# Performance work log

Hardware: AMD Instinct MI355X
Metric: run time of the kernel (lower is better)

## Reference

```python
import jax, jax.numpy as jnp
import numpy as np

B, S, E = 8, 2048, 1024
EPS = 1e-5

def _layernorm(x, w, b):
    mu = jnp.mean(x, axis=-1, keepdims=True)
    var = jnp.mean(jnp.square(x - mu), axis=-1, keepdims=True)
    return (x - mu) * jax.lax.rsqrt(var + EPS) * w + b

def setup_inputs() -> dict:
    key = jax.random.key(0)
    ks = jax.random.split(key, 12)
    x = jax.random.normal(ks[0], (B, S, E), dtype=jnp.float32)
    pad_mask = jax.random.randint(ks[1], (B, 1, S), 0, 2).astype(bool)
    pad_mask = pad_mask.at[:, :, 0].set(False)  # ensure no fully-masked row
    s = 1.0 / np.sqrt(E)
    Wq = jax.random.normal(ks[2], (E, E), jnp.float32) * s
    Wk = jax.random.normal(ks[3], (E, E), jnp.float32) * s
    Wv = jax.random.normal(ks[4], (E, E), jnp.float32) * s
    bq = jnp.zeros((E,), jnp.float32)
    bk = jnp.zeros((E,), jnp.float32)
    bv = jnp.zeros((E,), jnp.float32)
    W1 = jax.random.normal(ks[5], (2 * E, E), jnp.float32) * s
    b1 = jnp.zeros((2 * E,), jnp.float32)
    W2 = jax.random.normal(ks[6], (E, 2 * E), jnp.float32) * (1.0 / np.sqrt(2 * E))
    b2 = jnp.zeros((E,), jnp.float32)
    ln1_w = jnp.ones((E,), jnp.float32); ln1_b = jnp.zeros((E,), jnp.float32)
    ln2_w = jnp.ones((E,), jnp.float32); ln2_b = jnp.zeros((E,), jnp.float32)
    return {"x": x, "pad_mask": pad_mask, "ln1_w": ln1_w, "ln1_b": ln1_b,
            "ln2_w": ln2_w, "ln2_b": ln2_b, "Wq": Wq, "bq": bq, "Wk": Wk,
            "bk": bk, "Wv": Wv, "bv": bv, "W1": W1, "b1": b1, "W2": W2, "b2": b2}

def reference(x, pad_mask, ln1_w, ln1_b, ln2_w, ln2_b, Wq, bq, Wk, bk, Wv, bv, W1, b1, W2, b2):
    scale = jnp.sqrt(jnp.float32(x.shape[-1]))
    normed = _layernorm(x, ln1_w, ln1_b)
    Q = jnp.einsum('bse,de->bsd', normed, Wq) + bq
    K = jnp.einsum('bse,de->bsd', normed, Wk) + bk
    V = jnp.einsum('bse,de->bsd', normed, Wv) + bv
    scores = jnp.einsum('bqd,bkd->bqk', Q, K) / scale  # [B,S,S]
    scores = jnp.where(pad_mask, -jnp.inf, scores)
    attn = jax.nn.softmax(scores, axis=2)  # dropout is identity at inference
    x = x + jnp.einsum('bqk,bkd->bqd', attn, V)
    h = _layernorm(x, ln2_w, ln2_b)
    h = jax.nn.relu(jnp.einsum('bse,fe->bsf', h, W1) + b1)
    x = x + jnp.einsum('bsf,ef->bse', h, W2) + b2
    return x
```

## Files before the change

kernel.cpp:

```cpp
#include <hip/hip_runtime.h>
#include <hip/hip_bf16.h>
#include <cstdint>

#define B_ 8
#define S_ 2048
#define E_ 1024

using u16 = unsigned short;

typedef __bf16 bf16x8 __attribute__((ext_vector_type(8)));
typedef float f32x4 __attribute__((ext_vector_type(4)));

__device__ inline u16 f2bf(float f) {
  uint32_t u = __float_as_uint(f);
  uint32_t r = (u + 0x7fffu + ((u >> 16) & 1u)) >> 16;
  return (u16)r;
}

template<bool HAS_BIAS, bool RELU, bool HAS_RES, bool OUT_BF16, bool SCORES,
         bool GATHER_A, bool RUNTK>
__global__ __launch_bounds__(256) void gemm_nt(
    const u16* __restrict__ A, const u16* __restrict__ B, void* __restrict__ C,
    const float* __restrict__ bias, const float* __restrict__ res,
    int lda, int ldb, int ldc, int K,
    long long strideA, long long strideB, long long strideC,
    const int* __restrict__ cidx, const int* __restrict__ cnt)
{
  __shared__ u16 lA[128 * 32];
  __shared__ u16 lB[128 * 32];

  const int tid  = threadIdx.x;
  const int lane = tid & 63;
  const int wave = tid >> 6;

  const int GM = 4, GN = 8;
  const int nbn = gridDim.x, nbm = gridDim.y, nz = gridDim.z;
  int bm, bn, bz;
  {
    const int total = nbn * nbm * nz;
    const long long lin = blockIdx.x +
        (long long)nbn * (blockIdx.y + (long long)nbm * blockIdx.z);
    if ((nbm % GM) == 0 && (nbn % GN) == 0 && (total % (8 * GM * GN)) == 0) {
      const int xcd = (int)(lin & 7);
      const int loc = (int)(lin >> 3);
      const int sper = GM * GN;
      const int super = (loc / sper) * 8 + xcd;
      const int ins   = loc % sper;
      const int spz = (nbm / GM) * (nbn / GN);
      bz = super / spz;
      const int s2 = super % spz;
      const int sm = s2 % (nbm / GM);
      const int sn = s2 / (nbm / GM);
      bm = sm * GM + (ins % GM);
      bn = sn * GN + (ins / GM);
    } else { bm = blockIdx.y; bn = blockIdx.x; bz = blockIdx.z; }
  }

  int count = 0, cpad = 0;
  if (SCORES || GATHER_A || RUNTK) {
    count = cnt[bz * 2];
    cpad  = cnt[bz * 2 + 1];
    if (GATHER_A && bm * 128 >= cpad) return;
    if (SCORES   && bn * 128 >= cpad) return;
  }
  const int Keff = RUNTK ? cpad : K;

  const u16* Ab = A + (long long)bz * strideA;
  const u16* Bb = B + (long long)bz * strideB;

  const bool stageA = (wave < 2);
  const int  wpart  = (wave & 1) * 64;
  const int  srow   = lane >> 2;
  const int  scol   = (lane & 3) * 8;
  const int  ld     = stageA ? lda : ldb;

  long long goff[4];
  if (GATHER_A && stageA) {
    const int* cx = cidx;
#pragma unroll
    for (int c = 0; c < 4; ++c) {
      const int r = cx[(long long)bz * S_ + bm * 128 + wpart + 16 * c + srow];
      goff[c] = (long long)r * lda + scol;
    }
  } else {
    const int rbase = (stageA ? bm : bn) * 128 + wpart + srow;
#pragma unroll
    for (int c = 0; c < 4; ++c)
      goff[c] = (long long)(rbase + 16 * c) * ld + scol;
  }
  const u16* gb = stageA ? Ab : Bb;
  u16* ldst = (stageA ? lA : lB) + wpart * 32;

  f32x4 acc[4][4];
#pragma unroll
  for (int i = 0; i < 4; ++i)
#pragma unroll
    for (int j = 0; j < 4; ++j)
      acc[i][j] = (f32x4){0.f, 0.f, 0.f, 0.f};

  const int wm = (wave >> 1) * 64;
  const int wn = (wave & 1) * 64;
  const u16* pA = lA + (wm + (lane & 15)) * 32 + (lane >> 4) * 8;
  const u16* pB = lB + (wn + (lane & 15)) * 32 + (lane >> 4) * 8;

  const int nk = Keff >> 5;
  for (int kt = 0; kt < nk; ++kt) {
    __syncthreads();
#pragma unroll
    for (int c = 0; c < 4; ++c) {
      __builtin_amdgcn_global_load_lds(
          (const __attribute__((address_space(1))) void*)(gb + goff[c] + kt * 32),
          (__attribute__((address_space(3))) void*)(ldst + c * 16 * 32),
          16, 0, 0);
    }
    __syncthreads();

    bf16x8 af[4], bfr[4];
#pragma unroll
    for (int i = 0; i < 4; ++i) af[i] = *(const bf16x8*)(pA + i * 16 * 32);
#pragma unroll
    for (int j = 0; j < 4; ++j) bfr[j] = *(const bf16x8*)(pB + j * 16 * 32);
#pragma unroll
    for (int i = 0; i < 4; ++i)
#pragma unroll
      for (int j = 0; j < 4; ++j)
        acc[i][j] = __builtin_amdgcn_mfma_f32_16x16x32_bf16(af[i], bfr[j], acc[i][j], 0, 0, 0);
  }

  const int rb = wm + (lane >> 4) * 4;
  const int cb = wn + (lane & 15);
  const float* resb = (const float*)C;
  if (HAS_RES) resb = res + (long long)bz * strideC;
  u16*   cb16 = (u16*)C   + (long long)bz * strideC;
  float* cf32 = (float*)C + (long long)bz * strideC;

#pragma unroll
  for (int j = 0; j < 4; ++j) {
    const int gn = bn * 128 + cb + j * 16;
    const float bvv = HAS_BIAS ? bias[gn] : 0.f;
    const bool cmask = SCORES && (gn >= count);
#pragma unroll
    for (int i = 0; i < 4; ++i) {
#pragma unroll
      for (int r = 0; r < 4; ++r) {
        const int gm = bm * 128 + rb + i * 16 + r;
        const long long idx = (long long)gm * ldc + gn;
        float v = acc[i][j][r] + bvv;
        if (SCORES) { v *= 0.03125f; if (cmask) v = -3.0e38f; }
        if (RELU) v = fmaxf(v, 0.f);
        if (HAS_RES) v += resb[idx];
        if (OUT_BF16) cb16[idx] = f2bf(v);
        else          cf32[idx] = v;
      }
    }
  }
}

__global__ __launch_bounds__(256) void layernorm_kernel(
    const float* __restrict__ x, const float* __restrict__ w,
    const float* __restrict__ b, u16* __restrict__ out)
{
  const int row = blockIdx.x;
  const int tid = threadIdx.x;
  const float4 v = ((const float4*)(x + (long long)row * E_))[tid];
  float s  = v.x + v.y + v.z + v.w;
  float s2 = v.x * v.x + v.y * v.y + v.z * v.z + v.w * v.w;
#pragma unroll
  for (int o = 32; o >= 1; o >>= 1) { s += __shfl_xor(s, o); s2 += __shfl_xor(s2, o); }
  __shared__ float rs[4], rs2[4];
  const int wave = tid >> 6, lane = tid & 63;
  if (lane == 0) { rs[wave] = s; rs2[wave] = s2; }
  __syncthreads();
  s  = rs[0] + rs[1] + rs[2] + rs[3];
  s2 = rs2[0] + rs2[1] + rs2[2] + rs2[3];
  const float mu   = s * (1.f / E_);
  const float var  = s2 * (1.f / E_) - mu * mu;
  const float rstd = rsqrtf(var + 1e-5f);
  const float4 wv = ((const float4*)w)[tid];
  const float4 bv = ((const float4*)b)[tid];
  ushort4 o;
  o.x = f2bf((v.x - mu) * rstd * wv.x + bv.x);
  o.y = f2bf((v.y - mu) * rstd * wv.y + bv.y);
  o.z = f2bf((v.z - mu) * rstd * wv.z + bv.z);
  o.w = f2bf((v.w - mu) * rstd * wv.w + bv.w);
  ((ushort4*)(out + (long long)row * E_))[tid] = o;
}

__global__ __launch_bounds__(256) void softmax_bf16_kernel(
    u16* __restrict__ sp, const int* __restrict__ cnt)
{
  const int row = blockIdx.x;
  const int bz  = row >> 11;
  const int tid = threadIdx.x;
  const int cpad = cnt[bz * 2 + 1];
  const bool act = (tid * 8) < cpad;
  u16* pr = sp + (long long)row * S_;

  float v[8];
  if (act) {
    const uint4 raw = ((const uint4*)pr)[tid];
    const uint32_t w[4] = {raw.x, raw.y, raw.z, raw.w};
#pragma unroll
    for (int c = 0; c < 4; ++c) {
      v[2 * c]     = __uint_as_float(w[c] << 16);
      v[2 * c + 1] = __uint_as_float(w[c] & 0xffff0000u);
    }
  } else {
#pragma unroll
    for (int i = 0; i < 8; ++i) v[i] = -3.38e38f;
  }
  float mx = -3.38e38f;
#pragma unroll
  for (int i = 0; i < 8; ++i) mx = fmaxf(mx, v[i]);
#pragma unroll
  for (int o = 32; o >= 1; o >>= 1) mx = fmaxf(mx, __shfl_xor(mx, o));
  __shared__ float red[4];
  const int wave = tid >> 6, lane = tid & 63;
  if (lane == 0) red[wave] = mx;
  __syncthreads();
  mx = fmaxf(fmaxf(red[0], red[1]), fmaxf(red[2], red[3]));

  float s = 0.f;
#pragma unroll
  for (int i = 0; i < 8; ++i) { v[i] = __expf(v[i] - mx); s += v[i]; }
#pragma unroll
  for (int o = 32; o >= 1; o >>= 1) s += __shfl_xor(s, o);
  __syncthreads();
  if (lane == 0) red[wave] = s;
  __syncthreads();
  s = red[0] + red[1] + red[2] + red[3];
  const float inv = 1.f / s;

  if (act) {
    uint4 o4;
    uint32_t* ow = (uint32_t*)&o4;
#pragma unroll
    for (int c = 0; c < 4; ++c) {
      const uint32_t lo = f2bf(v[2 * c] * inv);
      const uint32_t hi = f2bf(v[2 * c + 1] * inv);
      ow[c] = lo | (hi << 16);
    }
    ((uint4*)pr)[tid] = o4;
  }
}

__global__ __launch_bounds__(256) void transpose_kernel(
    const u16* __restrict__ KVc, u16* __restrict__ Vt, const int* __restrict__ cnt)
{
  const int bl = blockIdx.z;
  const int s0 = blockIdx.y * 32;
  if (s0 >= cnt[bl * 2 + 1]) return;
  __shared__ u16 tile[32][33];
  const int e0 = blockIdx.x * 32;
  const int tx = threadIdx.x & 31, ty = threadIdx.x >> 5;
  const u16* src = KVc + ((long long)bl * S_ + s0) * (2 * E_) + E_ + e0;
#pragma unroll
  for (int r = 0; r < 32; r += 8)
    tile[ty + r][tx] = src[(long long)(ty + r) * (2 * E_) + tx];
  __syncthreads();
  u16* dst = Vt + ((long long)bl * E_ + e0) * S_ + s0;
#pragma unroll
  for (int r = 0; r < 32; r += 8)
    dst[(long long)(ty + r) * S_ + tx] = tile[tx][ty + r];
}

__global__ __launch_bounds__(256) void prep_kernel(
    const float* __restrict__ Wq, const float* __restrict__ Wk,
    const float* __restrict__ Wv, const float* __restrict__ W1,
    const float* __restrict__ W2, const float* __restrict__ bk,
    const float* __restrict__ bv,
    u16* __restrict__ Wqb, u16* __restrict__ Wkvb,
    u16* __restrict__ W1b, u16* __restrict__ W2b, float* __restrict__ bkv)
{
  const int N1 = E_ * E_;
  const long long i = (long long)blockIdx.x * 256 + threadIdx.x;
  if (i < N1)               Wqb[i] = f2bf(Wq[i]);
  else if (i < 2LL * N1)    Wkvb[i - N1] = f2bf(Wk[i - N1]);
  else if (i < 3LL * N1)    Wkvb[N1 + (i - 2LL * N1)] = f2bf(Wv[i - 2LL * N1]);
  else if (i < 5LL * N1)    W1b[i - 3LL * N1] = f2bf(W1[i - 3LL * N1]);
  else if (i < 7LL * N1)    W2b[i - 5LL * N1] = f2bf(W2[i - 5LL * N1]);
  else if (i < 7LL * N1 + 2 * E_) {
    const int j = (int)(i - 7LL * N1);
    bkv[j] = (j < E_) ? bk[j] : bv[j - E_];
  }
}

__global__ void detect_kernel(const unsigned char* __restrict__ m, int* __restrict__ flag)
{
  __shared__ int any;
  if (threadIdx.x == 0) any = 0;
  __syncthreads();
  int loc = 0;
  for (int i = threadIdx.x; i < B_ * S_; i += 256)
    if ((i & 3) && m[i]) loc = 1;
  if (loc) atomicOr(&any, 1);
  __syncthreads();
  if (threadIdx.x == 0) *flag = any;
}

__global__ __launch_bounds__(256) void compact_kernel(
    const void* __restrict__ mask, const int* __restrict__ flag,
    int* __restrict__ cidx, int* __restrict__ cnt)
{
  const int b = blockIdx.x;
  const int tid = threadIdx.x, lane = tid & 63, wave = tid >> 6;
  const bool u8m = (*flag != 0);
  const unsigned char* m8 = (const unsigned char*)mask + (long long)b * S_;
  const int* m32 = (const int*)mask + (long long)b * S_;

  int keep[8]; int my = 0;
#pragma unroll
  for (int j = 0; j < 8; ++j) {
    const int s = tid * 8 + j;
    const bool k = u8m ? (m8[s] == 0) : (m32[s] == 0);
    keep[j] = k ? 1 : 0; my += keep[j];
  }
  int pre = my;
#pragma unroll
  for (int o = 1; o < 64; o <<= 1) {
    const int n = __shfl_up(pre, o);
    if (lane >= o) pre += n;
  }
  __shared__ int wsum[4];
  if (lane == 63) wsum[wave] = pre;
  __syncthreads();
  int wbase = 0;
#pragma unroll
  for (int w = 0; w < 4; ++w) if (w < wave) wbase += wsum[w];
  int pos = wbase + pre - my;
  int* cx = cidx + (long long)b * S_;
#pragma unroll
  for (int j = 0; j < 8; ++j)
    if (keep[j]) cx[pos++] = tid * 8 + j;
  const int total = wsum[0] + wsum[1] + wsum[2] + wsum[3];
  const int cpad = (total + 127) & ~127;
  for (int i = total + tid; i < cpad; i += 256) cx[i] = 0;
  if (tid == 0) { cnt[b * 2] = total; cnt[b * 2 + 1] = cpad; }
}

extern "C" void kernel_launch(void* const* d_in, const int* in_sizes, int n_in,
                              void* d_out, int out_size, void* d_ws, size_t ws_size,
                              hipStream_t stream)
{
  const float* x    = (const float*)d_in[0];
  const void*  mask = d_in[1];
  const float* ln1w = (const float*)d_in[2];
  const float* ln1b = (const float*)d_in[3];
  const float* ln2w = (const float*)d_in[4];
  const float* ln2b = (const float*)d_in[5];
  const float* Wq   = (const float*)d_in[6];
  const float* bq   = (const float*)d_in[7];
  const float* Wk   = (const float*)d_in[8];
  const float* bk   = (const float*)d_in[9];
  const float* Wv   = (const float*)d_in[10];
  const float* bv   = (const float*)d_in[11];
  const float* W1   = (const float*)d_in[12];
  const float* b1   = (const float*)d_in[13];
  const float* W2   = (const float*)d_in[14];
  const float* b2   = (const float*)d_in[15];

  const size_t MB = 1024ull * 1024ull;
  char* p = (char*)d_ws;
  int* flag    = (int*)p;   p += 256;
  int* cnt     = (int*)p;   p += 256;
  int* cidx    = (int*)p;   p += (size_t)B_ * S_ * 4;
  u16* Wqb     = (u16*)p;   p += (size_t)E_ * E_ * 2;
  u16* Wkvb    = (u16*)p;   p += (size_t)2 * E_ * E_ * 2;
  u16* W1b     = (u16*)p;   p += (size_t)2 * E_ * E_ * 2;
  u16* W2b     = (u16*)p;   p += (size_t)2 * E_ * E_ * 2;
  float* bkv   = (float*)p; p += 2 * E_ * 4;
  u16* normedb = (u16*)p;   p += (size_t)B_ * S_ * E_ * 2;
  char* chunk  = p;
  const size_t used  = (size_t)(p - (char*)d_ws);
  const size_t avail = (ws_size > used) ? (ws_size - used) : 0;

  int bc = 1;
  for (int c = 8; c >= 1; c >>= 1)
    if (avail >= 24 * MB * (size_t)c) { bc = c; break; }

  float* out = (float*)d_out;
  dim3 blk(256);

  detect_kernel<<<1, 256, 0, stream>>>((const unsigned char*)mask, flag);
  compact_kernel<<<B_, blk, 0, stream>>>(mask, flag, cidx, cnt);
  {
    const long long tot = 7LL * E_ * E_ + 2 * E_;
    prep_kernel<<<(int)((tot + 255) / 256), blk, 0, stream>>>(
        Wq, Wk, Wv, W1, W2, bk, bv, Wqb, Wkvb, W1b, W2b, bkv);
  }

  layernorm_kernel<<<B_ * S_, blk, 0, stream>>>(x, ln1w, ln1b, normedb);

  for (int b0 = 0; b0 < B_; b0 += bc) {
    u16* Qc  = (u16*)chunk;
    u16* KVc = Qc + (size_t)bc * S_ * E_;
    u16* Vt  = KVc + (size_t)bc * S_ * 2 * E_;
    u16* Pc  = Vt + (size_t)bc * E_ * S_;
    const int* cntb  = cnt + b0 * 2;
    const int* cidxb = cidx + (size_t)b0 * S_;

    gemm_nt<true, false, false, true, false, false, false>
        <<<dim3(E_ / 128, bc * S_ / 128, 1), blk, 0, stream>>>(
        normedb + (size_t)b0 * S_ * E_, Wqb, Qc, bq, nullptr,
        E_, E_, E_, E_, 0, 0, 0, nullptr, nullptr);

    gemm_nt<true, false, false, true, false, true, false>
        <<<dim3(2 * E_ / 128, S_ / 128, bc), blk, 0, stream>>>(
        normedb + (size_t)b0 * S_ * E_, Wkvb, KVc, bkv, nullptr,
        E_, E_, 2 * E_, E_,
        (long long)S_ * E_, 0, (long long)S_ * 2 * E_, cidxb, cntb);

    transpose_kernel<<<dim3(E_ / 32, S_ / 32, bc), blk, 0, stream>>>(KVc, Vt, cntb);

    gemm_nt<false, false, false, true, true, false, false>
        <<<dim3(S_ / 128, S_ / 128, bc), blk, 0, stream>>>(
        Qc, KVc, Pc, nullptr, nullptr,
        E_, 2 * E_, S_, E_,
        (long long)S_ * E_, (long long)S_ * 2 * E_, (long long)S_ * S_,
        nullptr, cntb);

    softmax_bf16_kernel<<<bc * S_, blk, 0, stream>>>(Pc, cntb);

    gemm_nt<false, false, true, false, false, false, true>
        <<<dim3(E_ / 128, S_ / 128, bc), blk, 0, stream>>>(
        Pc, Vt, out + (size_t)b0 * S_ * E_, nullptr,
        x + (size_t)b0 * S_ * E_, S_, S_, E_, S_,
        (long long)S_ * S_, (long long)E_ * S_, (long long)S_ * E_,
        nullptr, cntb);
  }

  layernorm_kernel<<<B_ * S_, blk, 0, stream>>>(out, ln2w, ln2b, normedb);

  size_t mr_sz = avail / ((size_t)2 * E_ * 2);
  int mr = (int)((mr_sz > 16384) ? 16384 : mr_sz);
  mr &= ~127;
  if (mr < 128) mr = 128;
  u16* hb = (u16*)chunk;
  for (int m0 = 0; m0 < B_ * S_; m0 += mr) {
    const int mm = (B_ * S_ - m0 < mr) ? (B_ * S_ - m0) : mr;
    gemm_nt<true, true, false, true, false, false, false>
        <<<dim3((2 * E_) / 128, mm / 128, 1), blk, 0, stream>>>(
        normedb + (size_t)m0 * E_, W1b, hb, b1, nullptr,
        E_, E_, 2 * E_, E_, 0, 0, 0, nullptr, nullptr);
    gemm_nt<true, false, true, false, false, false, false>
        <<<dim3(E_ / 128, mm / 128, 1), blk, 0, stream>>>(
        hb, W2b, out + (size_t)m0 * E_, b2, out + (size_t)m0 * E_,
        2 * E_, 2 * E_, E_, 2 * E_, 0, 0, 0, nullptr, nullptr);
  }
}
```

Measured before the change: 778.1 us.

## Rewrite GEMM as 256x256 tile, 512-thread, double-buffered pipelined kernel with swizzled LDS

Replaces the 128x128x32 single-buffered GEMM with a 256x256x64 tile computed by 8 waves. LDS is double-buffered and XOR-swizzled, and global-to-LDS loads are interleaved with four MFMA phases using explicit barriers, waitcnt and setprio. The goal is higher arithmetic intensity, fewer bank conflicts and overlap of memory traffic with MFMA work. Padding for the compacted key count grows to 256, and all launch grids change to match. The cost is much higher LDS and register use, fewer blocks, and more wasted padding work.

```diff
diff --git a/kernel.cpp b/kernel.cpp
--- a/kernel.cpp
+++ b/kernel.cpp
@@ -19,21 +19,21 @@
 
 template<bool HAS_BIAS, bool RELU, bool HAS_RES, bool OUT_BF16, bool SCORES,
          bool GATHER_A, bool RUNTK>
-__global__ __launch_bounds__(256) void gemm_nt(
+__global__ __launch_bounds__(512, 2) void gemm_nt(
     const u16* __restrict__ A, const u16* __restrict__ B, void* __restrict__ C,
     const float* __restrict__ bias, const float* __restrict__ res,
     int lda, int ldb, int ldc, int K,
     long long strideA, long long strideB, long long strideC,
     const int* __restrict__ cidx, const int* __restrict__ cnt)
 {
-  __shared__ u16 lA[128 * 32];
-  __shared__ u16 lB[128 * 32];
+  __shared__ __attribute__((aligned(16))) u16 lA[2][2][128 * 64];
+  __shared__ __attribute__((aligned(16))) u16 lB[2][2][128 * 64];
 
   const int tid  = threadIdx.x;
   const int lane = tid & 63;
   const int wave = tid >> 6;
 
-  const int GM = 4, GN = 8;
+  const int GM = 8, GN = 4;
   const int nbn = gridDim.x, nbm = gridDim.y, nz = gridDim.z;
   int bm, bn, bz;
   {
@@ -60,92 +60,139 @@
   if (SCORES || GATHER_A || RUNTK) {
     count = cnt[bz * 2];
     cpad  = cnt[bz * 2 + 1];
-    if (GATHER_A && bm * 128 >= cpad) return;
-    if (SCORES   && bn * 128 >= cpad) return;
+    if (GATHER_A && bm * 256 >= cpad) return;
+    if (SCORES   && bn * 256 >= cpad) return;
   }
   const int Keff = RUNTK ? cpad : K;
+  const int nk = Keff >> 6;
 
   const u16* Ab = A + (long long)bz * strideA;
   const u16* Bb = B + (long long)bz * strideB;
 
-  const bool stageA = (wave < 2);
-  const int  wpart  = (wave & 1) * 64;
-  const int  srow   = lane >> 2;
-  const int  scol   = (lane & 3) * 8;
-  const int  ld     = stageA ? lda : ldb;
-
-  long long goff[4];
-  if (GATHER_A && stageA) {
-    const int* cx = cidx;
-#pragma unroll
-    for (int c = 0; c < 4; ++c) {
-      const int r = cx[(long long)bz * S_ + bm * 128 + wpart + 16 * c + srow];
-      goff[c] = (long long)r * lda + scol;
+  const int srow = tid >> 3;
+  const int scol = ((tid & 7) ^ (srow & 7)) * 8;
+  long long rowA[2][2], rowB[2][2];
+#pragma unroll
+  for (int h = 0; h < 2; ++h)
+#pragma unroll
+    for (int l = 0; l < 2; ++l) {
+      int ra = bm * 256 + h * 128 + srow + l * 64;
+      if (GATHER_A) ra = cidx[(long long)bz * S_ + ra];
+      rowA[h][l] = (long long)ra * lda + scol;
+      rowB[h][l] = (long long)(bn * 256 + h * 128 + srow + l * 64) * ldb + scol;
     }
-  } else {
-    const int rbase = (stageA ? bm : bn) * 128 + wpart + srow;
-#pragma unroll
-    for (int c = 0; c < 4; ++c)
-      goff[c] = (long long)(rbase + 16 * c) * ld + scol;
-  }
-  const u16* gb = stageA ? Ab : Bb;
-  u16* ldst = (stageA ? lA : lB) + wpart * 32;
-
-  f32x4 acc[4][4];
-#pragma unroll
-  for (int i = 0; i < 4; ++i)
-#pragma unroll
-    for (int j = 0; j < 4; ++j)
-      acc[i][j] = (f32x4){0.f, 0.f, 0.f, 0.f};
-
-  const int wm = (wave >> 1) * 64;
-  const int wn = (wave & 1) * 64;
-  const u16* pA = lA + (wm + (lane & 15)) * 32 + (lane >> 4) * 8;
-  const u16* pB = lB + (wn + (lane & 15)) * 32 + (lane >> 4) * 8;
-
-  const int nk = Keff >> 5;
-  for (int kt = 0; kt < nk; ++kt) {
-    __syncthreads();
-#pragma unroll
-    for (int c = 0; c < 4; ++c) {
-      __builtin_amdgcn_global_load_lds(
-          (const __attribute__((address_space(1))) void*)(gb + goff[c] + kt * 32),
-          (__attribute__((address_space(3))) void*)(ldst + c * 16 * 32),
-          16, 0, 0);
-    }
-    __syncthreads();
-
-    bf16x8 af[4], bfr[4];
-#pragma unroll
-    for (int i = 0; i < 4; ++i) af[i] = *(const bf16x8*)(pA + i * 16 * 32);
-#pragma unroll
-    for (int j = 0; j < 4; ++j) bfr[j] = *(const bf16x8*)(pB + j * 16 * 32);
-#pragma unroll
-    for (int i = 0; i < 4; ++i)
-#pragma unroll
-      for (int j = 0; j < 4; ++j)
-        acc[i][j] = __builtin_amdgcn_mfma_f32_16x16x32_bf16(af[i], bfr[j], acc[i][j], 0, 0, 0);
-  }
-
-  const int rb = wm + (lane >> 4) * 4;
-  const int cb = wn + (lane & 15);
+  const int ldsoff0 = tid * 8;
+  const int ldsoff1 = (tid + 512) * 8;
+
+  const int wr = wave >> 2, wc = wave & 3;
+  const int rA = wr * 64 + (lane & 15);
+  const int rB = wc * 32 + (lane & 15);
+  int aoff[2], boff[2];
+#pragma unroll
+  for (int k2 = 0; k2 < 2; ++k2) {
+    aoff[k2] = rA * 64 + (((k2 * 4 + (lane >> 4)) ^ (rA & 7)) * 8);
+    boff[k2] = rB * 64 + (((k2 * 4 + (lane >> 4)) ^ (rB & 7)) * 8);
+  }
+
+  f32x4 acc[2][2][4][2];
+#pragma unroll
+  for (int a = 0; a < 2; ++a)
+#pragma unroll
+    for (int b = 0; b < 2; ++b)
+#pragma unroll
+      for (int mi = 0; mi < 4; ++mi)
+#pragma unroll
+        for (int ni = 0; ni < 2; ++ni)
+          acc[a][b][mi][ni] = (f32x4){0.f, 0.f, 0.f, 0.f};
+
+#define STAGE_A(H, T) {                                                        \
+    const int tt_ = ((T) < nk) ? (T) : (nk - 1);                               \
+    __builtin_amdgcn_global_load_lds(                                          \
+        (const __attribute__((address_space(1))) void*)                        \
+            (Ab + rowA[H][0] + (long long)tt_ * 64),                           \
+        (__attribute__((address_space(3))) void*)(&lA[(T) & 1][H][ldsoff0]),   \
+        16, 0, 0);                                                             \
+    __builtin_amdgcn_global_load_lds(                                          \
+        (const __attribute__((address_space(1))) void*)                        \
+            (Ab + rowA[H][1] + (long long)tt_ * 64),                           \
+        (__attribute__((address_space(3))) void*)(&lA[(T) & 1][H][ldsoff1]),   \
+        16, 0, 0); }
+
+#define STAGE_B(H, T) {                                                        \
+    const int tt_ = ((T) < nk) ? (T) : (nk - 1);                               \
+    __builtin_amdgcn_global_load_lds(                                          \
+        (const __attribute__((address_space(1))) void*)                        \
+            (Bb + rowB[H][0] + (long long)tt_ * 64),                           \
+        (__attribute__((address_space(3))) void*)(&lB[(T) & 1][H][ldsoff0]),   \
+        16, 0, 0);                                                             \
+    __builtin_amdgcn_global_load_lds(                                          \
+        (const __attribute__((address_space(1))) void*)                        \
+            (Bb + rowB[H][1] + (long long)tt_ * 64),                           \
+        (__attribute__((address_space(3))) void*)(&lB[(T) & 1][H][ldsoff1]),   \
+        16, 0, 0); }
+
+#define PHASE(MH, NH, STG, DO_VM) {                                            \
+    bf16x8 af[4][2], bfv[2][2];                                                \
+    const u16* pa_ = &lA[buf][MH][0];                                          \
+    const u16* pb_ = &lB[buf][NH][0];                                          \
+    _Pragma("unroll") for (int mi = 0; mi < 4; ++mi)                           \
+      _Pragma("unroll") for (int k2 = 0; k2 < 2; ++k2)                         \
+        af[mi][k2] = *(const bf16x8*)(pa_ + mi * 1024 + aoff[k2]);             \
+    _Pragma("unroll") for (int ni = 0; ni < 2; ++ni)                           \
+      _Pragma("unroll") for (int k2 = 0; k2 < 2; ++k2)                         \
+        bfv[ni][k2] = *(const bf16x8*)(pb_ + ni * 1024 + boff[k2]);            \
+    STG;                                                                       \
+    __builtin_amdgcn_s_barrier();                                              \
+    asm volatile("s_waitcnt lgkmcnt(0)" ::: "memory");                         \
+    __builtin_amdgcn_s_setprio(1);                                             \
+    _Pragma("unroll") for (int mi = 0; mi < 4; ++mi)                           \
+      _Pragma("unroll") for (int ni = 0; ni < 2; ++ni)                         \
+        _Pragma("unroll") for (int k2 = 0; k2 < 2; ++k2)                       \
+          acc[MH][NH][mi][ni] = __builtin_amdgcn_mfma_f32_16x16x32_bf16(       \
+              af[mi][k2], bfv[ni][k2], acc[MH][NH][mi][ni], 0, 0, 0);          \
+    __builtin_amdgcn_s_setprio(0);                                             \
+    if (DO_VM) asm volatile("s_waitcnt vmcnt(4)" ::: "memory");                \
+    __builtin_amdgcn_s_barrier(); }
+
+  STAGE_A(0, 0); STAGE_B(0, 0); STAGE_A(1, 0); STAGE_B(1, 0);
+  STAGE_A(0, 1); STAGE_B(1, 1);
+  asm volatile("s_waitcnt vmcnt(4)" ::: "memory");
+  __builtin_amdgcn_s_barrier();
+
+  int buf = 0;
+  for (int t = 0; t < nk; ++t, buf ^= 1) {
+    PHASE(0, 0, STAGE_A(1, t + 1), false)
+    PHASE(0, 1, STAGE_B(0, t + 1), false)
+    PHASE(1, 1, STAGE_A(0, t + 2), false)
+    PHASE(1, 0, STAGE_B(1, t + 2), true)
+  }
+  asm volatile("s_waitcnt vmcnt(0)" ::: "memory");
+
+#undef PHASE
+#undef STAGE_A
+#undef STAGE_B
+
   const float* resb = (const float*)C;
   if (HAS_RES) resb = res + (long long)bz * strideC;
   u16*   cb16 = (u16*)C   + (long long)bz * strideC;
   float* cf32 = (float*)C + (long long)bz * strideC;
 
 #pragma unroll
-  for (int j = 0; j < 4; ++j) {
-    const int gn = bn * 128 + cb + j * 16;
+  for (int mh = 0; mh < 2; ++mh)
+#pragma unroll
+  for (int nh = 0; nh < 2; ++nh)
+#pragma unroll
+  for (int ni = 0; ni < 2; ++ni) {
+    const int gn = bn * 256 + nh * 128 + wc * 32 + ni * 16 + (lane & 15);
     const float bvv = HAS_BIAS ? bias[gn] : 0.f;
     const bool cmask = SCORES && (gn >= count);
 #pragma unroll
-    for (int i = 0; i < 4; ++i) {
+    for (int mi = 0; mi < 4; ++mi) {
 #pragma unroll
       for (int r = 0; r < 4; ++r) {
-        const int gm = bm * 128 + rb + i * 16 + r;
+        const int gm = bm * 256 + mh * 128 + wr * 64 + mi * 16 + (lane >> 4) * 4 + r;
         const long long idx = (long long)gm * ldc + gn;
-        float v = acc[i][j][r] + bvv;
+        float v = acc[mh][nh][mi][ni][r] + bvv;
         if (SCORES) { v *= 0.03125f; if (cmask) v = -3.0e38f; }
         if (RELU) v = fmaxf(v, 0.f);
         if (HAS_RES) v += resb[idx];
@@ -333,7 +380,7 @@
   for (int j = 0; j < 8; ++j)
     if (keep[j]) cx[pos++] = tid * 8 + j;
   const int total = wsum[0] + wsum[1] + wsum[2] + wsum[3];
-  const int cpad = (total + 127) & ~127;
+  const int cpad = (total + 255) & ~255;
   for (int i = total + tid; i < cpad; i += 256) cx[i] = 0;
   if (tid == 0) { cnt[b * 2] = total; cnt[b * 2 + 1] = cpad; }
 }
@@ -380,6 +427,7 @@
 
   float* out = (float*)d_out;
   dim3 blk(256);
+  dim3 blkg(512);
 
   detect_kernel<<<1, 256, 0, stream>>>((const unsigned char*)mask, flag);
   compact_kernel<<<B_, blk, 0, stream>>>(mask, flag, cidx, cnt);
@@ -400,12 +448,12 @@
     const int* cidxb = cidx + (size_t)b0 * S_;
 
     gemm_nt<true, false, false, true, false, false, false>
-        <<<dim3(E_ / 128, bc * S_ / 128, 1), blk, 0, stream>>>(
+        <<<dim3(E_ / 256, bc * S_ / 256, 1), blkg, 0, stream>>>(
         normedb + (size_t)b0 * S_ * E_, Wqb, Qc, bq, nullptr,
         E_, E_, E_, E_, 0, 0, 0, nullptr, nullptr);
 
     gemm_nt<true, false, false, true, false, true, false>
-        <<<dim3(2 * E_ / 128, S_ / 128, bc), blk, 0, stream>>>(
+        <<<dim3(2 * E_ / 256, S_ / 256, bc), blkg, 0, stream>>>(
         normedb + (size_t)b0 * S_ * E_, Wkvb, KVc, bkv, nullptr,
         E_, E_, 2 * E_, E_,
         (long long)S_ * E_, 0, (long long)S_ * 2 * E_, cidxb, cntb);
@@ -413,7 +461,7 @@
     transpose_kernel<<<dim3(E_ / 32, S_ / 32, bc), blk, 0, stream>>>(KVc, Vt, cntb);
 
     gemm_nt<false, false, false, true, true, false, false>
-        <<<dim3(S_ / 128, S_ / 128, bc), blk, 0, stream>>>(
+        <<<dim3(S_ / 256, S_ / 256, bc), blkg, 0, stream>>>(
         Qc, KVc, Pc, nullptr, nullptr,
         E_, 2 * E_, S_, E_,
         (long long)S_ * E_, (long long)S_ * 2 * E_, (long long)S_ * S_,
@@ -422,7 +470,7 @@
     softmax_bf16_kernel<<<bc * S_, blk, 0, stream>>>(Pc, cntb);
 
     gemm_nt<false, false, true, false, false, false, true>
-        <<<dim3(E_ / 128, S_ / 128, bc), blk, 0, stream>>>(
+        <<<dim3(E_ / 256, S_ / 256, bc), blkg, 0, stream>>>(
         Pc, Vt, out + (size_t)b0 * S_ * E_, nullptr,
         x + (size_t)b0 * S_ * E_, S_, S_, E_, S_,
         (long long)S_ * S_, (long long)E_ * S_, (long long)S_ * E_,
@@ -433,17 +481,17 @@
 
   size_t mr_sz = avail / ((size_t)2 * E_ * 2);
   int mr = (int)((mr_sz > 16384) ? 16384 : mr_sz);
-  mr &= ~127;
-  if (mr < 128) mr = 128;
+  mr &= ~255;
+  if (mr < 256) mr = 256;
   u16* hb = (u16*)chunk;
   for (int m0 = 0; m0 < B_ * S_; m0 += mr) {
     const int mm = (B_ * S_ - m0 < mr) ? (B_ * S_ - m0) : mr;
     gemm_nt<true, true, false, true, false, false, false>
-        <<<dim3((2 * E_) / 128, mm / 128, 1), blk, 0, stream>>>(
+        <<<dim3((2 * E_) / 256, mm / 256, 1), blkg, 0, stream>>>(
         normedb + (size_t)m0 * E_, W1b, hb, b1, nullptr,
         E_, E_, 2 * E_, E_, 0, 0, 0, nullptr, nullptr);
     gemm_nt<true, false, true, false, false, false, false>
-        <<<dim3(E_ / 128, mm / 128, 1), blk, 0, stream>>>(
+        <<<dim3(E_ / 256, mm / 256, 1), blkg, 0, stream>>>(
         hb, W2b, out + (size_t)m0 * E_, b2, out + (size_t)m0 * E_,
         2 * E_, 2 * E_, E_, 2 * E_, 0, 0, 0, nullptr, nullptr);
   }
```

New measurement: 718.1 us. 7.7% less time.

## Double-buffer GEMM LDS with BK=64, XOR swizzle and hand-scheduled MFMA

Applied to the files above, without the earlier changes.

Rewrites the GEMM main loop to use a K-tile of 64 with two LDS buffers. The next tile is prefetched by global_load_lds while the current one is consumed, which removes one of the two barriers per iteration. LDS columns are XOR-swizzled to avoid bank conflicts, and fragment reads use explicit ds_read_b128 with staged lgkmcnt waits interleaved with the MFMAs. The change also sets launch_bounds occupancy to 2 and swaps the block-grouping shape to 8x4. It adds LDS pressure (64KB per block) and relies on inline asm wait counts being correct.

```diff
diff --git a/kernel.cpp b/kernel.cpp
--- a/kernel.cpp
+++ b/kernel.cpp
@@ -19,21 +19,21 @@
 
 template<bool HAS_BIAS, bool RELU, bool HAS_RES, bool OUT_BF16, bool SCORES,
          bool GATHER_A, bool RUNTK>
-__global__ __launch_bounds__(256) void gemm_nt(
+__global__ __launch_bounds__(256, 2) void gemm_nt(
     const u16* __restrict__ A, const u16* __restrict__ B, void* __restrict__ C,
     const float* __restrict__ bias, const float* __restrict__ res,
     int lda, int ldb, int ldc, int K,
     long long strideA, long long strideB, long long strideC,
     const int* __restrict__ cidx, const int* __restrict__ cnt)
 {
-  __shared__ u16 lA[128 * 32];
-  __shared__ u16 lB[128 * 32];
+  __shared__ __attribute__((aligned(16))) u16 lA[2][128 * 64];
+  __shared__ __attribute__((aligned(16))) u16 lB[2][128 * 64];
 
   const int tid  = threadIdx.x;
   const int lane = tid & 63;
   const int wave = tid >> 6;
 
-  const int GM = 4, GN = 8;
+  const int GM = 8, GN = 4;
   const int nbn = gridDim.x, nbm = gridDim.y, nz = gridDim.z;
   int bm, bn, bz;
   {
@@ -64,88 +64,124 @@
     if (SCORES   && bn * 128 >= cpad) return;
   }
   const int Keff = RUNTK ? cpad : K;
+  const int nk = Keff >> 6;
 
   const u16* Ab = A + (long long)bz * strideA;
   const u16* Bb = B + (long long)bz * strideB;
 
-  const bool stageA = (wave < 2);
-  const int  wpart  = (wave & 1) * 64;
-  const int  srow   = lane >> 2;
-  const int  scol   = (lane & 3) * 8;
-  const int  ld     = stageA ? lda : ldb;
-
-  long long goff[4];
-  if (GATHER_A && stageA) {
-    const int* cx = cidx;
-#pragma unroll
-    for (int c = 0; c < 4; ++c) {
-      const int r = cx[(long long)bz * S_ + bm * 128 + wpart + 16 * c + srow];
-      goff[c] = (long long)r * lda + scol;
-    }
-  } else {
-    const int rbase = (stageA ? bm : bn) * 128 + wpart + srow;
-#pragma unroll
-    for (int c = 0; c < 4; ++c)
-      goff[c] = (long long)(rbase + 16 * c) * ld + scol;
-  }
-  const u16* gb = stageA ? Ab : Bb;
-  u16* ldst = (stageA ? lA : lB) + wpart * 32;
+  const int srow = tid >> 3;
+  const int scol = ((tid & 7) ^ (srow & 7)) * 8;
+  long long rowA[4], rowB[4];
+#pragma unroll
+  for (int l = 0; l < 4; ++l) {
+    int ra = bm * 128 + srow + l * 32;
+    if (GATHER_A) ra = cidx[(long long)bz * S_ + ra];
+    rowA[l] = (long long)ra * lda + scol;
+    rowB[l] = (long long)(bn * 128 + srow + l * 32) * ldb + scol;
+  }
+  const int ldsoff = tid * 8;
+
+  const int wr = wave >> 1, wc = wave & 1;
+  const int rA = wr * 64 + (lane & 15);
+  const int rB = wc * 64 + (lane & 15);
+#define LDSP3(P) ((uint32_t)(uintptr_t)(__attribute__((address_space(3))) const void*)(P))
+  uint32_t aA0 = LDSP3(&lA[0][0]) +
+      2u * (uint32_t)(rA * 64 + (((0 * 4 + (lane >> 4)) ^ (rA & 7)) * 8));
+  uint32_t aA1 = LDSP3(&lA[0][0]) +
+      2u * (uint32_t)(rA * 64 + (((1 * 4 + (lane >> 4)) ^ (rA & 7)) * 8));
+  uint32_t bB0 = LDSP3(&lB[0][0]) +
+      2u * (uint32_t)(rB * 64 + (((0 * 4 + (lane >> 4)) ^ (rB & 7)) * 8));
+  uint32_t bB1 = LDSP3(&lB[0][0]) +
+      2u * (uint32_t)(rB * 64 + (((1 * 4 + (lane >> 4)) ^ (rB & 7)) * 8));
+#undef LDSP3
 
   f32x4 acc[4][4];
 #pragma unroll
-  for (int i = 0; i < 4; ++i)
-#pragma unroll
-    for (int j = 0; j < 4; ++j)
-      acc[i][j] = (f32x4){0.f, 0.f, 0.f, 0.f};
-
-  const int wm = (wave >> 1) * 64;
-  const int wn = (wave & 1) * 64;
-  const u16* pA = lA + (wm + (lane & 15)) * 32 + (lane >> 4) * 8;
-  const u16* pB = lB + (wn + (lane & 15)) * 32 + (lane >> 4) * 8;
-
-  const int nk = Keff >> 5;
-  for (int kt = 0; kt < nk; ++kt) {
-    __syncthreads();
-#pragma unroll
-    for (int c = 0; c < 4; ++c) {
-      __builtin_amdgcn_global_load_lds(
-          (const __attribute__((address_space(1))) void*)(gb + goff[c] + kt * 32),
-          (__attribute__((address_space(3))) void*)(ldst + c * 16 * 32),
-          16, 0, 0);
-    }
-    __syncthreads();
-
-    bf16x8 af[4], bfr[4];
-#pragma unroll
-    for (int i = 0; i < 4; ++i) af[i] = *(const bf16x8*)(pA + i * 16 * 32);
-#pragma unroll
-    for (int j = 0; j < 4; ++j) bfr[j] = *(const bf16x8*)(pB + j * 16 * 32);
-#pragma unroll
-    for (int i = 0; i < 4; ++i)
-#pragma unroll
-      for (int j = 0; j < 4; ++j)
-        acc[i][j] = __builtin_amdgcn_mfma_f32_16x16x32_bf16(af[i], bfr[j], acc[i][j], 0, 0, 0);
-  }
-
-  const int rb = wm + (lane >> 4) * 4;
-  const int cb = wn + (lane & 15);
+  for (int mi = 0; mi < 4; ++mi)
+#pragma unroll
+    for (int ni = 0; ni < 4; ++ni)
+      acc[mi][ni] = (f32x4){0.f, 0.f, 0.f, 0.f};
+
+#define STAGE(T) {                                                             \
+    const int tt_ = ((T) < nk) ? (T) : (nk - 1);                               \
+    _Pragma("unroll") for (int l = 0; l < 4; ++l)                              \
+      __builtin_amdgcn_global_load_lds(                                        \
+          (const __attribute__((address_space(1))) void*)                      \
+              (Ab + rowA[l] + (long long)tt_ * 64),                            \
+          (__attribute__((address_space(3))) void*)                            \
+              (&lA[(T) & 1][l * 2048 + ldsoff]),                               \
+          16, 0, 0);                                                           \
+    _Pragma("unroll") for (int l = 0; l < 4; ++l)                              \
+      __builtin_amdgcn_global_load_lds(                                        \
+          (const __attribute__((address_space(1))) void*)                      \
+              (Bb + rowB[l] + (long long)tt_ * 64),                            \
+          (__attribute__((address_space(3))) void*)                            \
+              (&lB[(T) & 1][l * 2048 + ldsoff]),                               \
+          16, 0, 0); }
+
+#define DSR(D, ADDR, OFF) \
+    asm volatile("ds_read_b128 %0, %1 offset:" OFF : "=v"(D) : "v"(ADDR))
+#define LGKM(NSTR) asm volatile("s_waitcnt lgkmcnt(" NSTR ")" ::: "memory")
+#define SCHED0()   __builtin_amdgcn_sched_barrier(0)
+#define BAR()      __builtin_amdgcn_s_barrier()
+
+#define MFMA_NI(NI) {                                                          \
+    _Pragma("unroll") for (int mi = 0; mi < 4; ++mi)                           \
+      _Pragma("unroll") for (int k2 = 0; k2 < 2; ++k2)                         \
+        acc[mi][NI] = __builtin_amdgcn_mfma_f32_16x16x32_bf16(                 \
+            af[mi][k2], bf[NI][k2], acc[mi][NI], 0, 0, 0); }
+
+  STAGE(0);
+  asm volatile("s_waitcnt vmcnt(0)" ::: "memory");
+  BAR();
+
+  bf16x8 af[4][2], bf[4][2];
+  for (int t = 0; t < nk; ++t) {
+    STAGE(t + 1);
+    DSR(af[0][0], aA0, "0");     DSR(af[0][1], aA1, "0");
+    DSR(af[1][0], aA0, "2048");  DSR(af[1][1], aA1, "2048");
+    DSR(af[2][0], aA0, "4096");  DSR(af[2][1], aA1, "4096");
+    DSR(af[3][0], aA0, "6144");  DSR(af[3][1], aA1, "6144");
+    DSR(bf[0][0], bB0, "0");     DSR(bf[0][1], bB1, "0");
+    DSR(bf[1][0], bB0, "2048");  DSR(bf[1][1], bB1, "2048");
+    DSR(bf[2][0], bB0, "4096");  DSR(bf[2][1], bB1, "4096");
+    DSR(bf[3][0], bB0, "6144");  DSR(bf[3][1], bB1, "6144");
+    __builtin_amdgcn_s_setprio(1);
+    LGKM("6"); SCHED0(); MFMA_NI(0);
+    LGKM("4"); SCHED0(); MFMA_NI(1);
+    LGKM("2"); SCHED0(); MFMA_NI(2);
+    LGKM("0"); SCHED0(); MFMA_NI(3);
+    __builtin_amdgcn_s_setprio(0);
+    asm volatile("s_waitcnt vmcnt(0)" ::: "memory");
+    BAR();
+    const uint32_t d = (t & 1) ? (uint32_t)-16384 : 16384u;
+    aA0 += d; aA1 += d; bB0 += d; bB1 += d;
+  }
+
+#undef MFMA_NI
+#undef DSR
+#undef STAGE
+#undef BAR
+#undef LGKM
+#undef SCHED0
+
   const float* resb = (const float*)C;
   if (HAS_RES) resb = res + (long long)bz * strideC;
   u16*   cb16 = (u16*)C   + (long long)bz * strideC;
   float* cf32 = (float*)C + (long long)bz * strideC;
 
 #pragma unroll
-  for (int j = 0; j < 4; ++j) {
-    const int gn = bn * 128 + cb + j * 16;
+  for (int ni = 0; ni < 4; ++ni) {
+    const int gn = bn * 128 + wc * 64 + ni * 16 + (lane & 15);
     const float bvv = HAS_BIAS ? bias[gn] : 0.f;
     const bool cmask = SCORES && (gn >= count);
 #pragma unroll
-    for (int i = 0; i < 4; ++i) {
+    for (int mi = 0; mi < 4; ++mi) {
 #pragma unroll
       for (int r = 0; r < 4; ++r) {
-        const int gm = bm * 128 + rb + i * 16 + r;
+        const int gm = bm * 128 + wr * 64 + mi * 16 + (lane >> 4) * 4 + r;
         const long long idx = (long long)gm * ldc + gn;
-        float v = acc[i][j][r] + bvv;
+        float v = acc[mi][ni][r] + bvv;
         if (SCORES) { v *= 0.03125f; if (cmask) v = -3.0e38f; }
         if (RELU) v = fmaxf(v, 0.f);
         if (HAS_RES) v += resb[idx];
@@ -380,6 +416,7 @@
 
   float* out = (float*)d_out;
   dim3 blk(256);
+  dim3 blkg(256);
 
   detect_kernel<<<1, 256, 0, stream>>>((const unsigned char*)mask, flag);
   compact_kernel<<<B_, blk, 0, stream>>>(mask, flag, cidx, cnt);
@@ -400,12 +437,12 @@
     const int* cidxb = cidx + (size_t)b0 * S_;
 
     gemm_nt<true, false, false, true, false, false, false>
-        <<<dim3(E_ / 128, bc * S_ / 128, 1), blk, 0, stream>>>(
+        <<<dim3(E_ / 128, bc * S_ / 128, 1), blkg, 0, stream>>>(
         normedb + (size_t)b0 * S_ * E_, Wqb, Qc, bq, nullptr,
         E_, E_, E_, E_, 0, 0, 0, nullptr, nullptr);
 
     gemm_nt<true, false, false, true, false, true, false>
-        <<<dim3(2 * E_ / 128, S_ / 128, bc), blk, 0, stream>>>(
+        <<<dim3(2 * E_ / 128, S_ / 128, bc), blkg, 0, stream>>>(
         normedb + (size_t)b0 * S_ * E_, Wkvb, KVc, bkv, nullptr,
         E_, E_, 2 * E_, E_,
         (long long)S_ * E_, 0, (long long)S_ * 2 * E_, cidxb, cntb);
@@ -413,7 +450,7 @@
     transpose_kernel<<<dim3(E_ / 32, S_ / 32, bc), blk, 0, stream>>>(KVc, Vt, cntb);
 
     gemm_nt<false, false, false, true, true, false, false>
-        <<<dim3(S_ / 128, S_ / 128, bc), blk, 0, stream>>>(
+        <<<dim3(S_ / 128, S_ / 128, bc), blkg, 0, stream>>>(
         Qc, KVc, Pc, nullptr, nullptr,
         E_, 2 * E_, S_, E_,
         (long long)S_ * E_, (long long)S_ * 2 * E_, (long long)S_ * S_,
@@ -422,7 +459,7 @@
     softmax_bf16_kernel<<<bc * S_, blk, 0, stream>>>(Pc, cntb);
 
     gemm_nt<false, false, true, false, false, false, true>
-        <<<dim3(E_ / 128, S_ / 128, bc), blk, 0, stream>>>(
+        <<<dim3(E_ / 128, S_ / 128, bc), blkg, 0, stream>>>(
         Pc, Vt, out + (size_t)b0 * S_ * E_, nullptr,
         x + (size_t)b0 * S_ * E_, S_, S_, E_, S_,
         (long long)S_ * S_, (long long)E_ * S_, (long long)S_ * E_,
@@ -439,11 +476,11 @@
   for (int m0 = 0; m0 < B_ * S_; m0 += mr) {
     const int mm = (B_ * S_ - m0 < mr) ? (B_ * S_ - m0) : mr;
     gemm_nt<true, true, false, true, false, false, false>
-        <<<dim3((2 * E_) / 128, mm / 128, 1), blk, 0, stream>>>(
+        <<<dim3((2 * E_) / 128, mm / 128, 1), blkg, 0, stream>>>(
         normedb + (size_t)m0 * E_, W1b, hb, b1, nullptr,
         E_, E_, 2 * E_, E_, 0, 0, 0, nullptr, nullptr);
     gemm_nt<true, false, true, false, false, false, false>
-        <<<dim3(E_ / 128, mm / 128, 1), blk, 0, stream>>>(
+        <<<dim3(E_ / 128, mm / 128, 1), blkg, 0, stream>>>(
         hb, W2b, out + (size_t)m0 * E_, b2, out + (size_t)m0 * E_,
         2 * E_, 2 * E_, E_, 2 * E_, 0, 0, 0, nullptr, nullptr);
   }
```

Measured after the change: 652.3 us. -16.2%, faster.
